# Optimization experiments

Measured on AMD Instinct MI355X. Metric: run time of the kernel, lower is better.

## Reference

```python
import jax, jax.numpy as jnp
import numpy as np

D_MODEL = 1024
N_HEADS = 16
D_K = D_MODEL // N_HEADS
BATCH = 4
SEQ = 2048


def setup_inputs() -> dict:
    key = jax.random.key(0)
    ks = jax.random.split(key, 12)
    s = 1.0 / np.sqrt(D_MODEL)
    inp = {
        "query": jax.random.normal(ks[0], (BATCH, SEQ, D_MODEL), jnp.float32),
        "key": jax.random.normal(ks[1], (BATCH, SEQ, D_MODEL), jnp.float32),
        "value": jax.random.normal(ks[2], (BATCH, SEQ, D_MODEL), jnp.float32),
        # causal mask: True = masked (ignored), broadcastable over batch/heads
        "mask": jnp.triu(jnp.ones((SEQ, SEQ), bool), k=1)[None, None, :, :],
        "w_q": jax.random.normal(ks[3], (D_MODEL, D_MODEL), jnp.float32) * s,
        "b_q": jax.random.normal(ks[4], (D_MODEL,), jnp.float32) * s,
        "w_k": jax.random.normal(ks[5], (D_MODEL, D_MODEL), jnp.float32) * s,
        "b_k": jax.random.normal(ks[6], (D_MODEL,), jnp.float32) * s,
        "w_v": jax.random.normal(ks[7], (D_MODEL, D_MODEL), jnp.float32) * s,
        "b_v": jax.random.normal(ks[8], (D_MODEL,), jnp.float32) * s,
        "w_o": jax.random.normal(ks[9], (D_MODEL, D_MODEL), jnp.float32) * s,
        "b_o": jax.random.normal(ks[10], (D_MODEL,), jnp.float32) * s,
    }
    return inp


def _split_heads(x):
    # (B, S, D) -> (B, H, S, d_k)
    b, s, _ = x.shape
    return x.reshape(b, s, N_HEADS, D_K).transpose(0, 2, 1, 3)


def reference(query, key, value, mask, w_q, b_q, w_k, b_k, w_v, b_v, w_o, b_o):
    # torch Linear: y = x @ W.T + b
    q = _split_heads(query @ w_q.T + b_q)
    k = _split_heads(key @ w_k.T + b_k)
    v = _split_heads(value @ w_v.T + b_v)
    scale = 1.0 / jnp.sqrt(jnp.asarray(D_K, q.dtype))
    scores = jnp.einsum("bhqd,bhkd->bhqk", q, k) * scale
    scores = jnp.where(mask, jnp.asarray(-jnp.inf, scores.dtype), scores)
    weights = jax.nn.softmax(scores, axis=-1)  # dropout p=0.0 (eval)
    attn = jnp.einsum("bhqk,bhkd->bhqd", weights, v)
    b = attn.shape[0]
    attn = attn.transpose(0, 2, 1, 3).reshape(b, -1, D_MODEL)
    return attn @ w_o.T + b_o
```

## Files before the change

### kernel.cpp

```cpp
#include <hip/hip_runtime.h>

#define S_LEN 2048
#define DMODEL 1024
#define H_CNT 16
#define DK 64
#define BATCH 4

typedef __attribute__((ext_vector_type(8))) short short8;
typedef __attribute__((ext_vector_type(4))) float f32x4;
typedef __attribute__((ext_vector_type(16))) float f32x16;

static __device__ __forceinline__ short f2bf(float f) {
  union { float f; unsigned u; } x; x.f = f;
  unsigned r = x.u + 0x7fffu + ((x.u >> 16) & 1u);
  return (short)(r >> 16);
}

static __device__ __forceinline__ unsigned cvt_pk_bf16(float lo, float hi) {
  unsigned r;
  asm("v_cvt_pk_bf16_f32 %0, %1, %2" : "=v"(r) : "v"(lo), "v"(hi));
  return r;
}

__global__ __launch_bounds__(256) void cast_kernel(const float* __restrict__ src,
                                                   short* __restrict__ dst, int n8) {
  int i = blockIdx.x * 256 + threadIdx.x;
  if (i >= n8) return;
  const float4* s4 = (const float4*)src;
  float4 a = s4[2 * i], b = s4[2 * i + 1];
  short8 o;
  o[0] = f2bf(a.x); o[1] = f2bf(a.y); o[2] = f2bf(a.z); o[3] = f2bf(a.w);
  o[4] = f2bf(b.x); o[5] = f2bf(b.y); o[6] = f2bf(b.z); o[7] = f2bf(b.w);
  ((short8*)dst)[i] = o;
}

template <int MODE>
__global__ __launch_bounds__(256) void gemm_bt(const short* __restrict__ A,
                                               const short* __restrict__ B,
                                               const float* __restrict__ bias,
                                               void* __restrict__ Cout,
                                               int M, int N, int K, float scl) {
  __shared__ short As[128][32];
  __shared__ short Bs[128][32];
  const int tid = threadIdx.x;
  const int lane = tid & 63, wid = tid >> 6;
  const int m0 = blockIdx.y * 128, n0 = blockIdx.x * 128;
  const int wr = (wid >> 1) * 64, wc = (wid & 1) * 64;
  const int lrow = lane & 15, lk8 = (lane >> 4) * 8;
  const int sr = tid >> 2, sk = (tid & 3) * 8;

  f32x4 acc[4][4] = {};

  for (int k0 = 0; k0 < K; k0 += 32) {
    *(short8*)(&As[sr][sk])      = *(const short8*)(&A[(size_t)(m0 + sr) * K + k0 + sk]);
    *(short8*)(&As[sr + 64][sk]) = *(const short8*)(&A[(size_t)(m0 + sr + 64) * K + k0 + sk]);
    *(short8*)(&Bs[sr][sk])      = *(const short8*)(&B[(size_t)(n0 + sr) * K + k0 + sk]);
    *(short8*)(&Bs[sr + 64][sk]) = *(const short8*)(&B[(size_t)(n0 + sr + 64) * K + k0 + sk]);
    __syncthreads();
    short8 af[4], bfr[4];
#pragma unroll
    for (int m = 0; m < 4; m++) af[m] = *(const short8*)(&As[wr + m * 16 + lrow][lk8]);
#pragma unroll
    for (int n = 0; n < 4; n++) bfr[n] = *(const short8*)(&Bs[wc + n * 16 + lrow][lk8]);
#pragma unroll
    for (int m = 0; m < 4; m++)
#pragma unroll
      for (int n = 0; n < 4; n++)
        acc[m][n] = __builtin_amdgcn_mfma_f32_16x16x32_bf16(af[m], bfr[n], acc[m][n], 0, 0, 0);
    __syncthreads();
  }

#pragma unroll
  for (int n = 0; n < 4; n++) {
    int col = n0 + wc + n * 16 + lrow;
    float bv = bias[col];
#pragma unroll
    for (int m = 0; m < 4; m++) {
      int rbase = m0 + wr + m * 16 + (lane >> 4) * 4;
#pragma unroll
      for (int i = 0; i < 4; i++) {
        int row = rbase + i;
        float val = (acc[m][n][i] + bv) * scl;
        if (MODE == 2) {
          ((float*)Cout)[(size_t)row * N + col] = val;
        } else {
          int b = row >> 11, s2 = row & 2047, h = col >> 6, d = col & 63;
          short* o = (short*)Cout;
          if (MODE == 0)
            o[((size_t)(b * H_CNT + h) * S_LEN + s2) * DK + d] = f2bf(val);
          else
            o[((size_t)(b * H_CNT + h) * DK + d) * S_LEN + s2] = f2bf(val);
        }
      }
    }
  }
}

__global__ __launch_bounds__(256, 4) void attn2_kernel(const short* __restrict__ Q,
                                                       const short* __restrict__ Kc,
                                                       const short* __restrict__ Vt,
                                                       short* __restrict__ Oout) {
  const int bh = blockIdx.y;
  const int j = blockIdx.x;
  const int wid = threadIdx.x >> 6, lane = threadIdx.x & 63;
  const int qt = (wid == 0) ? j : (wid == 1) ? (31 - j) : (wid == 2) ? (32 + j) : (63 - j);
  const int q0 = qt * 32;
  const int ql = lane & 31, hl = lane >> 5;

  const short* Qb = Q + (size_t)bh * S_LEN * DK;
  const short* Kb = Kc + (size_t)bh * S_LEN * DK;
  const short* Vb = Vt + (size_t)bh * DK * S_LEN;

  short8 qf[4];
#pragma unroll
  for (int kk = 0; kk < 4; kk++)
    qf[kk] = *(const short8*)(&Qb[(q0 + ql) * DK + kk * 16 + hl * 8]);

  f32x16 oacc[2] = {};
  float mr = -1e30f, lr = 0.f;

  const int ntiles = qt + 1;
  for (int t = 0; t < ntiles; t++) {
    const int kv0 = t * 32;
    f32x16 st = {};
#pragma unroll
    for (int kk = 0; kk < 4; kk++) {
      short8 kf = *(const short8*)(&Kb[(kv0 + ql) * DK + kk * 16 + hl * 8]);
      st = __builtin_amdgcn_mfma_f32_32x32x16_bf16(kf, qf[kk], st, 0, 0, 0);
    }
    short8 vf[2][2];
#pragma unroll
    for (int td = 0; td < 2; td++)
#pragma unroll
      for (int kk = 0; kk < 2; kk++)
        vf[td][kk] = *(const short8*)(&Vb[(size_t)(td * 32 + ql) * S_LEN + kv0 + kk * 16 + hl * 8]);

    float p[16];
#pragma unroll
    for (int r = 0; r < 16; r++) p[r] = st[r];
    if (t == ntiles - 1) {
#pragma unroll
      for (int r = 0; r < 16; r++) {
        int kvr = (r & 3) + 8 * (r >> 2) + 4 * hl;
        if (kvr > ql) p[r] = -1e30f;
      }
    }
    float pm = p[0];
#pragma unroll
    for (int r = 1; r < 16; r++) pm = fmaxf(pm, p[r]);
    pm = fmaxf(pm, __shfl_xor(pm, 32, 64));
    if (!__all(pm <= mr + 8.f)) {
      float mnew = fmaxf(mr, pm);
      float al = __builtin_amdgcn_exp2f(mr - mnew);
      lr *= al;
#pragma unroll
      for (int td = 0; td < 2; td++)
#pragma unroll
        for (int r = 0; r < 16; r++) oacc[td][r] *= al;
      mr = mnew;
    }
    float rs = 0.f;
#pragma unroll
    for (int r = 0; r < 16; r++) {
      p[r] = __builtin_amdgcn_exp2f(p[r] - mr);
      rs += p[r];
    }
    rs += __shfl_xor(rs, 32, 64);
    lr += rs;

    unsigned w[8];
#pragma unroll
    for (int tt = 0; tt < 8; tt++) w[tt] = cvt_pk_bf16(p[2 * tt], p[2 * tt + 1]);
    union { short8 s; unsigned u[4]; } bf0, bf1;
    {
      unsigned xa = __shfl_xor((int)w[2], 32, 64), xb = __shfl_xor((int)w[0], 32, 64);
      bf0.u[0] = hl ? xa : w[0];
      bf0.u[2] = hl ? w[2] : xb;
    }
    {
      unsigned xa = __shfl_xor((int)w[3], 32, 64), xb = __shfl_xor((int)w[1], 32, 64);
      bf0.u[1] = hl ? xa : w[1];
      bf0.u[3] = hl ? w[3] : xb;
    }
    {
      unsigned xa = __shfl_xor((int)w[6], 32, 64), xb = __shfl_xor((int)w[4], 32, 64);
      bf1.u[0] = hl ? xa : w[4];
      bf1.u[2] = hl ? w[6] : xb;
    }
    {
      unsigned xa = __shfl_xor((int)w[7], 32, 64), xb = __shfl_xor((int)w[5], 32, 64);
      bf1.u[1] = hl ? xa : w[5];
      bf1.u[3] = hl ? w[7] : xb;
    }

#pragma unroll
    for (int td = 0; td < 2; td++) {
      oacc[td] = __builtin_amdgcn_mfma_f32_32x32x16_bf16(vf[td][0], bf0.s, oacc[td], 0, 0, 0);
      oacc[td] = __builtin_amdgcn_mfma_f32_32x32x16_bf16(vf[td][1], bf1.s, oacc[td], 0, 0, 0);
    }
  }

  const float inv = __builtin_amdgcn_rcpf(lr);
  const int b = bh >> 4, h = bh & 15;
  unsigned* ob = (unsigned*)Oout + ((size_t)b * S_LEN + q0 + ql) * (DMODEL / 2) + h * (DK / 2);
#pragma unroll
  for (int td = 0; td < 2; td++)
#pragma unroll
    for (int tt = 0; tt < 8; tt++) {
      unsigned pkv = cvt_pk_bf16(oacc[td][2 * tt] * inv, oacc[td][2 * tt + 1] * inv);
      ob[td * 16 + (tt & 1) + 4 * (tt >> 1) + 2 * hl] = pkv;
    }
}

extern "C" void kernel_launch(void* const* d_in, const int* in_sizes, int n_in,
                              void* d_out, int out_size, void* d_ws, size_t ws_size,
                              hipStream_t stream) {
  (void)in_sizes; (void)n_in; (void)out_size; (void)ws_size;
  const float* query = (const float*)d_in[0];
  const float* key_i = (const float*)d_in[1];
  const float* value = (const float*)d_in[2];
  const float* w_q = (const float*)d_in[4];
  const float* b_q = (const float*)d_in[5];
  const float* w_k = (const float*)d_in[6];
  const float* b_k = (const float*)d_in[7];
  const float* w_v = (const float*)d_in[8];
  const float* b_v = (const float*)d_in[9];
  const float* w_o = (const float*)d_in[10];
  const float* b_o = (const float*)d_in[11];

  const size_t XE = (size_t)BATCH * S_LEN * DMODEL;
  const size_t WE = (size_t)DMODEL * DMODEL;

  short* xq = (short*)d_ws;
  short* xk = xq + XE;
  short* xv = xk + XE;
  short* wq = xv + XE;
  short* wk = wq + WE;
  short* wv = wk + WE;
  short* wo = wv + WE;
  short* qb = wo + WE;
  short* kb = qb + XE;
  short* vtb = kb + XE;
  short* attnb = xq;

  const int M = BATCH * S_LEN;

  int n8x = (int)(XE / 8), n8w = (int)(WE / 8);
  cast_kernel<<<dim3((n8x + 255) / 256), 256, 0, stream>>>(query, xq, n8x);
  cast_kernel<<<dim3((n8x + 255) / 256), 256, 0, stream>>>(key_i, xk, n8x);
  cast_kernel<<<dim3((n8x + 255) / 256), 256, 0, stream>>>(value, xv, n8x);
  cast_kernel<<<dim3((n8w + 255) / 256), 256, 0, stream>>>(w_q, wq, n8w);
  cast_kernel<<<dim3((n8w + 255) / 256), 256, 0, stream>>>(w_k, wk, n8w);
  cast_kernel<<<dim3((n8w + 255) / 256), 256, 0, stream>>>(w_v, wv, n8w);
  cast_kernel<<<dim3((n8w + 255) / 256), 256, 0, stream>>>(w_o, wo, n8w);

  const float qscale = 0.125f * 1.44269504088896f;

  dim3 gg(DMODEL / 128, M / 128);
  gemm_bt<0><<<gg, 256, 0, stream>>>(xq, wq, b_q, qb, M, DMODEL, DMODEL, qscale);
  gemm_bt<0><<<gg, 256, 0, stream>>>(xk, wk, b_k, kb, M, DMODEL, DMODEL, 1.f);
  gemm_bt<1><<<gg, 256, 0, stream>>>(xv, wv, b_v, vtb, M, DMODEL, DMODEL, 1.f);

  attn2_kernel<<<dim3(16, BATCH * H_CNT), 256, 0, stream>>>(qb, kb, vtb, attnb);

  gemm_bt<2><<<gg, 256, 0, stream>>>(attnb, wo, b_o, d_out, M, DMODEL, DMODEL, 1.f);
}
```

Baseline: 302.0 us.

## Restructure projection GEMMs with direct global-to-LDS loads, 128x64 tiles, swizzled grid

```diff
diff --git a/kernel.cpp b/kernel.cpp
--- a/kernel.cpp
+++ b/kernel.cpp
@@ -20,6 +20,11 @@
   unsigned r;
   asm("v_cvt_pk_bf16_f32 %0, %1, %2" : "=v"(r) : "v"(lo), "v"(hi));
   return r;
+}
+
+static __device__ __forceinline__ void gl_lds16(const short* g, short* l) {
+  __builtin_amdgcn_global_load_lds((const __attribute__((address_space(1))) void*)g,
+                                   (__attribute__((address_space(3))) void*)l, 16, 0, 0);
 }
 
 __global__ __launch_bounds__(256) void cast_kernel(const float* __restrict__ src,
@@ -40,56 +45,69 @@
                                                const float* __restrict__ bias,
                                                void* __restrict__ Cout,
                                                int M, int N, int K, float scl) {
-  __shared__ short As[128][32];
-  __shared__ short Bs[128][32];
+  __shared__ short Sab[(128 + 64) * 32];
   const int tid = threadIdx.x;
   const int lane = tid & 63, wid = tid >> 6;
-  const int m0 = blockIdx.y * 128, n0 = blockIdx.x * 128;
-  const int wr = (wid >> 1) * 64, wc = (wid & 1) * 64;
+  const int lin = blockIdx.x;
+  const int w = (lin & 7) * 128 + (lin >> 3);
+  int bx, by;
+  if (MODE == 1) { bx = w >> 3; by = w & 7; }
+  else           { bx = w & 15; by = w >> 4; }
+  const int m0 = by * 128, n0 = bx * 64;
+  const int wr = wid * 32;
   const int lrow = lane & 15, lk8 = (lane >> 4) * 8;
-  const int sr = tid >> 2, sk = (tid & 3) * 8;
-
-  f32x4 acc[4][4] = {};
+
+  const int l4 = lane >> 2, lc = (lane & 3) * 8;
+  const short* gsrc[3];
+  short* ldst[3];
+#pragma unroll
+  for (int i = 0; i < 3; i++) {
+    int c = wid * 3 + i;
+    ldst[i] = &Sab[c * 512];
+    if (c < 8) gsrc[i] = &A[(size_t)(m0 + c * 16 + l4) * K + lc];
+    else       gsrc[i] = &B[(size_t)(n0 + (c - 8) * 16 + l4) * K + lc];
+  }
+
+  f32x4 acc[2][4] = {};
 
   for (int k0 = 0; k0 < K; k0 += 32) {
-    *(short8*)(&As[sr][sk])      = *(const short8*)(&A[(size_t)(m0 + sr) * K + k0 + sk]);
-    *(short8*)(&As[sr + 64][sk]) = *(const short8*)(&A[(size_t)(m0 + sr + 64) * K + k0 + sk]);
-    *(short8*)(&Bs[sr][sk])      = *(const short8*)(&B[(size_t)(n0 + sr) * K + k0 + sk]);
-    *(short8*)(&Bs[sr + 64][sk]) = *(const short8*)(&B[(size_t)(n0 + sr + 64) * K + k0 + sk]);
+#pragma unroll
+    for (int i = 0; i < 3; i++) gl_lds16(gsrc[i] + k0, ldst[i]);
     __syncthreads();
-    short8 af[4], bfr[4];
-#pragma unroll
-    for (int m = 0; m < 4; m++) af[m] = *(const short8*)(&As[wr + m * 16 + lrow][lk8]);
-#pragma unroll
-    for (int n = 0; n < 4; n++) bfr[n] = *(const short8*)(&Bs[wc + n * 16 + lrow][lk8]);
-#pragma unroll
-    for (int m = 0; m < 4; m++)
+    short8 af[2], bfr[4];
+#pragma unroll
+    for (int m = 0; m < 2; m++) af[m] = *(const short8*)(&Sab[(wr + m * 16 + lrow) * 32 + lk8]);
+#pragma unroll
+    for (int n = 0; n < 4; n++) bfr[n] = *(const short8*)(&Sab[(128 + n * 16 + lrow) * 32 + lk8]);
+#pragma unroll
+    for (int m = 0; m < 2; m++)
 #pragma unroll
       for (int n = 0; n < 4; n++)
         acc[m][n] = __builtin_amdgcn_mfma_f32_16x16x32_bf16(af[m], bfr[n], acc[m][n], 0, 0, 0);
     __syncthreads();
   }
 
+  const int g4 = (lane >> 4) * 4;
 #pragma unroll
   for (int n = 0; n < 4; n++) {
-    int col = n0 + wc + n * 16 + lrow;
-    float bv = bias[col];
-#pragma unroll
-    for (int m = 0; m < 4; m++) {
-      int rbase = m0 + wr + m * 16 + (lane >> 4) * 4;
+    const int col = n0 + n * 16 + lrow;
+#pragma unroll
+    for (int m = 0; m < 2; m++) {
 #pragma unroll
       for (int i = 0; i < 4; i++) {
-        int row = rbase + i;
-        float val = (acc[m][n][i] + bv) * scl;
-        if (MODE == 2) {
+        const int row = m0 + wr + m * 16 + g4 + i;
+        float val = acc[m][n][i];
+        if (MODE == 0) {
+          val = (val + bias[col]) * scl;
+          int b = row >> 11, s2 = row & 2047, h = col >> 6, d = col & 63;
+          ((short*)Cout)[((size_t)(b * H_CNT + h) * S_LEN + s2) * DK + d] = f2bf(val);
+        } else if (MODE == 1) {
+          val = val + bias[row];
+          int h = row >> 6, d = row & 63, b = col >> 11, s2 = col & 2047;
+          ((short*)Cout)[((size_t)(b * H_CNT + h) * DK + d) * S_LEN + s2] = f2bf(val);
+        } else {
+          val = val + bias[col];
           ((float*)Cout)[(size_t)row * N + col] = val;
-        } else {
-          int b = row >> 11, s2 = row & 2047, h = col >> 6, d = col & 63;
-          short* o = (short*)Cout;
-          if (MODE == 0)
-            o[((size_t)(b * H_CNT + h) * S_LEN + s2) * DK + d] = f2bf(val);
-          else
-            o[((size_t)(b * H_CNT + h) * DK + d) * S_LEN + s2] = f2bf(val);
         }
       }
     }
@@ -168,29 +186,29 @@
     rs += __shfl_xor(rs, 32, 64);
     lr += rs;
 
-    unsigned w[8];
-#pragma unroll
-    for (int tt = 0; tt < 8; tt++) w[tt] = cvt_pk_bf16(p[2 * tt], p[2 * tt + 1]);
+    unsigned wpk[8];
+#pragma unroll
+    for (int tt = 0; tt < 8; tt++) wpk[tt] = cvt_pk_bf16(p[2 * tt], p[2 * tt + 1]);
     union { short8 s; unsigned u[4]; } bf0, bf1;
     {
-      unsigned xa = __shfl_xor((int)w[2], 32, 64), xb = __shfl_xor((int)w[0], 32, 64);
-      bf0.u[0] = hl ? xa : w[0];
-      bf0.u[2] = hl ? w[2] : xb;
-    }
-    {
-      unsigned xa = __shfl_xor((int)w[3], 32, 64), xb = __shfl_xor((int)w[1], 32, 64);
-      bf0.u[1] = hl ? xa : w[1];
-      bf0.u[3] = hl ? w[3] : xb;
-    }
-    {
-      unsigned xa = __shfl_xor((int)w[6], 32, 64), xb = __shfl_xor((int)w[4], 32, 64);
-      bf1.u[0] = hl ? xa : w[4];
-      bf1.u[2] = hl ? w[6] : xb;
-    }
-    {
-      unsigned xa = __shfl_xor((int)w[7], 32, 64), xb = __shfl_xor((int)w[5], 32, 64);
-      bf1.u[1] = hl ? xa : w[5];
-      bf1.u[3] = hl ? w[7] : xb;
+      unsigned xa = __shfl_xor((int)wpk[2], 32, 64), xb = __shfl_xor((int)wpk[0], 32, 64);
+      bf0.u[0] = hl ? xa : wpk[0];
+      bf0.u[2] = hl ? wpk[2] : xb;
+    }
+    {
+      unsigned xa = __shfl_xor((int)wpk[3], 32, 64), xb = __shfl_xor((int)wpk[1], 32, 64);
+      bf0.u[1] = hl ? xa : wpk[1];
+      bf0.u[3] = hl ? wpk[3] : xb;
+    }
+    {
+      unsigned xa = __shfl_xor((int)wpk[6], 32, 64), xb = __shfl_xor((int)wpk[4], 32, 64);
+      bf1.u[0] = hl ? xa : wpk[4];
+      bf1.u[2] = hl ? wpk[6] : xb;
+    }
+    {
+      unsigned xa = __shfl_xor((int)wpk[7], 32, 64), xb = __shfl_xor((int)wpk[5], 32, 64);
+      bf1.u[1] = hl ? xa : wpk[5];
+      bf1.u[3] = hl ? wpk[7] : xb;
     }
 
 #pragma unroll
@@ -256,12 +274,11 @@
 
   const float qscale = 0.125f * 1.44269504088896f;
 
-  dim3 gg(DMODEL / 128, M / 128);
-  gemm_bt<0><<<gg, 256, 0, stream>>>(xq, wq, b_q, qb, M, DMODEL, DMODEL, qscale);
-  gemm_bt<0><<<gg, 256, 0, stream>>>(xk, wk, b_k, kb, M, DMODEL, DMODEL, 1.f);
-  gemm_bt<1><<<gg, 256, 0, stream>>>(xv, wv, b_v, vtb, M, DMODEL, DMODEL, 1.f);
+  gemm_bt<0><<<1024, 256, 0, stream>>>(xq, wq, b_q, qb, M, DMODEL, DMODEL, qscale);
+  gemm_bt<0><<<1024, 256, 0, stream>>>(xk, wk, b_k, kb, M, DMODEL, DMODEL, 1.f);
+  gemm_bt<1><<<1024, 256, 0, stream>>>(wv, xv, b_v, vtb, DMODEL, M, DMODEL, 1.f);
 
   attn2_kernel<<<dim3(16, BATCH * H_CNT), 256, 0, stream>>>(qb, kb, vtb, attnb);
 
-  gemm_bt<2><<<gg, 256, 0, stream>>>(attnb, wo, b_o, d_out, M, DMODEL, DMODEL, 1.f);
-}
+  gemm_bt<2><<<1024, 256, 0, stream>>>(attnb, wo, b_o, d_out, M, DMODEL, DMODEL, 1.f);
+}
```

Result: faster. 278.0 us (-8.0%).
